# Performance work log

Hardware: AMD Instinct MI355X
Metric: run time of the kernel (lower is better)

Reference implementation:

```python
import jax, jax.numpy as jnp
import numpy as np

N = 30000      # nodes
E = 480000     # edges (before self-loops)
IN = 128       # in_dim
HID = 256      # hidden_dim
HEADS = 4
C = HID // HEADS  # per-head channels = 64
NEG_SLOPE = 0.2


def setup_inputs() -> dict:
    key = jax.random.key(0)
    ks = jax.random.split(key, 12)
    s_in = 1.0 / np.sqrt(IN)
    s_h = 1.0 / np.sqrt(HID)
    return {
        "x": jax.random.normal(ks[0], (N, IN), dtype=jnp.float32),
        "edge_index": jax.random.randint(ks[1], (2, E), 0, N, dtype=jnp.int32),
        # GAT layer 1 (in: IN -> HEADS*C)
        "W1": jax.random.normal(ks[2], (IN, HID), dtype=jnp.float32) * s_in,
        "att_src1": jax.random.normal(ks[3], (HEADS, C), dtype=jnp.float32) * s_h,
        "att_dst1": jax.random.normal(ks[4], (HEADS, C), dtype=jnp.float32) * s_h,
        "b1": jnp.zeros((HID,), dtype=jnp.float32),
        # GAT layer 2 (in: HID -> HEADS*C)
        "W2": jax.random.normal(ks[5], (HID, HID), dtype=jnp.float32) * s_h,
        "att_src2": jax.random.normal(ks[6], (HEADS, C), dtype=jnp.float32) * s_h,
        "att_dst2": jax.random.normal(ks[7], (HEADS, C), dtype=jnp.float32) * s_h,
        "b2": jnp.zeros((HID,), dtype=jnp.float32),
        # LayerNorms
        "g1": jnp.ones((HID,), dtype=jnp.float32),
        "be1": jnp.zeros((HID,), dtype=jnp.float32),
        "g2": jnp.ones((HID,), dtype=jnp.float32),
        "be2": jnp.zeros((HID,), dtype=jnp.float32),
        # residual projection (in_dim != hidden_dim)
        "Wp": jax.random.normal(ks[8], (IN, HID), dtype=jnp.float32) * s_in,
        "bp": jnp.zeros((HID,), dtype=jnp.float32),
    }


def layer_norm(x, g, b, eps=1e-5):
    mu = jnp.mean(x, axis=-1, keepdims=True)
    var = jnp.var(x, axis=-1, keepdims=True)
    return (x - mu) * jax.lax.rsqrt(var + eps) * g + b


def gat_conv(x, src, dst, W, a_src, a_dst, bias):
    """PyG-style GATConv (concat heads). src/dst already include self-loops."""
    n = x.shape[0]
    h = (x @ W).reshape(n, HEADS, C)                     # (N, H, C)
    e_src = jnp.sum(h * a_src, axis=-1)                  # (N, H)
    e_dst = jnp.sum(h * a_dst, axis=-1)                  # (N, H)
    e = jax.nn.leaky_relu(e_src[src] + e_dst[dst], NEG_SLOPE)  # (Etot, H)
    # per-destination segment softmax (numerically stable)
    e_max = jax.lax.stop_gradient(jax.ops.segment_max(e, dst, num_segments=n))
    p = jnp.exp(e - e_max[dst])
    denom = jax.ops.segment_sum(p, dst, num_segments=n)[dst]
    alpha = p / denom                                    # (Etot, H)
    out = jax.ops.segment_sum(h[src] * alpha[..., None], dst, num_segments=n)
    return out.reshape(n, HID) + bias


def reference(x, edge_index, W1, att_src1, att_dst1, b1, W2, att_src2, att_dst2, b2,
              g1, be1, g2, be2, Wp, bp):
    n = x.shape[0]
    loop = jnp.arange(n, dtype=edge_index.dtype)
    src = jnp.concatenate([edge_index[0], loop])
    dst = jnp.concatenate([edge_index[1], loop])

    residual = x @ Wp + bp                               # proj residual
    h = gat_conv(x, src, dst, W1, att_src1, att_dst1, b1)
    h = jax.nn.elu(layer_norm(h + residual, g1, be1))
    # dropout is identity at inference
    residual = h
    h2 = gat_conv(h, src, dst, W2, att_src2, att_dst2, b2)
    out = jax.nn.elu(layer_norm(h2 + residual, g2, be2))
    return out
```

## Files before the change

kernel.cpp:

```cpp
#include <hip/hip_runtime.h>
#include <cstdint>
#include <cstddef>

#define N_NODES 30000
#define E_EDGES 480000
#define ETOT    510000
#define IN_DIM  128
#define HID     256
#define HEADS   4
#define NEG_SLOPE 0.2f
#define DEG_BLOCKS 1993
#define GEMM1_BX 235

static inline int cdiv(int a, int b){ return (a + b - 1) / b; }

typedef short bf16x8 __attribute__((ext_vector_type(8)));
typedef float f32x4  __attribute__((ext_vector_type(4)));
typedef float f32x2  __attribute__((ext_vector_type(2)));

__device__ __forceinline__ unsigned short f2bf(float f) {
  unsigned u = __float_as_uint(f);
  unsigned r = (u + 0x7FFFu + ((u >> 16) & 1u)) >> 16;
  return (unsigned short)r;
}
__device__ __forceinline__ float bf2f(unsigned short s) {
  return __uint_as_float((unsigned)s << 16);
}
__device__ __forceinline__ unsigned char f2fp8(float v) {
  return (unsigned char)(__builtin_amdgcn_cvt_pk_fp8_f32(v, v, 0, false) & 0xFF);
}

__global__ __launch_bounds__(256) void zero_deg(int4* __restrict__ deg4)
{
  deg4[blockIdx.x * 256 + threadIdx.x] = int4{0, 0, 0, 0};
}

__global__ __launch_bounds__(256) void setup(
    const int* __restrict__ ei, int* __restrict__ deg,
    const float* __restrict__ x, const float* __restrict__ W1,
    const float* __restrict__ Wp, const float* __restrict__ W2,
    ushort* __restrict__ xbf, ushort* __restrict__ w1t,
    ushort* __restrict__ wpt, ushort* __restrict__ w2t)
{
  int b = blockIdx.x;
  int t = threadIdx.x;
  if (b < DEG_BLOCKS) {
    int e = b * 256 + t;
    if (e < ETOT) {
      int d = (e < E_EDGES) ? ei[E_EDGES + e] : (e - E_EDGES);
      atomicAdd(&deg[d], 1);
    }
    return;
  }
  b -= DEG_BLOCKS;
  if (b < 3750) {
    int i = b * 256 + t;
    float4 v = ((const float4*)x)[i];
    ushort4 o;
    o.x = f2bf(v.x); o.y = f2bf(v.y); o.z = f2bf(v.z); o.w = f2bf(v.w);
    ((ushort4*)xbf)[i] = o;
  } else if (b < 3750 + 128) {
    int k = b - 3750;
    w1t[(size_t)t * IN_DIM + k] = f2bf(W1[(size_t)k * HID + t]);
  } else if (b < 3750 + 256) {
    int k = b - 3878;
    wpt[(size_t)t * IN_DIM + k] = f2bf(Wp[(size_t)k * HID + t]);
  } else {
    int k = b - 4006;
    w2t[(size_t)t * HID + k] = f2bf(W2[(size_t)k * HID + t]);
  }
}

template<int K, bool L1>
__device__ __forceinline__ void gemm_body(
    int bx, int by,
    const ushort* __restrict__ A,
    const ushort* __restrict__ WT,
    const float* __restrict__ att_src, const float* __restrict__ att_dst,
    unsigned char* __restrict__ hout, float* __restrict__ esrc, float* __restrict__ edst,
    ushort* __restrict__ rout, const float* __restrict__ pbias, int n)
{
  const int wave = threadIdx.x >> 6;
  const int lane = threadIdx.x & 63;
  const int wr = wave >> 1, wc = wave & 1;
  const int brow = bx * 128 + wr * 64;
  const int bcol = by * 128 + wc * 64;
  const int lrow = lane & 15;
  const int kgrp = lane >> 4;

  f32x4 acc[4][4] = {};
  for (int k0 = 0; k0 < K; k0 += 32) {
    const int kb = k0 + kgrp * 8;
    bf16x8 a[4], b[4];
    #pragma unroll
    for (int mi = 0; mi < 4; ++mi) {
      int r = brow + mi * 16 + lrow;
      r = min(r, n - 1);
      a[mi] = *(const bf16x8*)&A[(size_t)r * K + kb];
    }
    #pragma unroll
    for (int ni = 0; ni < 4; ++ni) {
      int c = bcol + ni * 16 + lrow;
      b[ni] = *(const bf16x8*)&WT[(size_t)c * K + kb];
    }
    #pragma unroll
    for (int mi = 0; mi < 4; ++mi)
      #pragma unroll
      for (int ni = 0; ni < 4; ++ni)
        acc[mi][ni] = __builtin_amdgcn_mfma_f32_16x16x32_bf16(a[mi], b[ni], acc[mi][ni], 0, 0, 0);
  }
  const bool proj = L1 && (bcol >= 256);
  #pragma unroll
  for (int mi = 0; mi < 4; ++mi) {
    #pragma unroll
    for (int r = 0; r < 4; ++r) {
      int row = brow + mi * 16 + kgrp * 4 + r;
      if (row < n) {
        #pragma unroll
        for (int ni = 0; ni < 4; ++ni) {
          int colg = bcol + ni * 16 + lrow;
          float v = acc[mi][ni][r];
          if (proj) {
            int c = colg - 256;
            rout[(size_t)row * HID + c] = f2bf(v + pbias[c]);
          } else {
            hout[(size_t)row * HID + colg] = f2fp8(v);
          }
        }
      }
    }
  }
  if (!proj) {
    const int hh = bcol >> 6;
    float as[4], ad[4];
    #pragma unroll
    for (int ni = 0; ni < 4; ++ni) {
      as[ni] = att_src[hh * 64 + ni * 16 + lrow];
      ad[ni] = att_dst[hh * 64 + ni * 16 + lrow];
    }
    #pragma unroll
    for (int mi = 0; mi < 4; ++mi) {
      #pragma unroll
      for (int r = 0; r < 4; ++r) {
        float vs = 0.f, vd = 0.f;
        #pragma unroll
        for (int ni = 0; ni < 4; ++ni) {
          float c = acc[mi][ni][r];
          vs += c * as[ni];
          vd += c * ad[ni];
        }
        #pragma unroll
        for (int m = 1; m <= 8; m <<= 1) {
          vs += __shfl_xor(vs, m);
          vd += __shfl_xor(vd, m);
        }
        int row = brow + mi * 16 + kgrp * 4 + r;
        if (lrow == 0 && row < n) {
          esrc[row * HEADS + hh] = vs;
          edst[row * HEADS + hh] = vd;
        }
      }
    }
  }
}

__global__ __launch_bounds__(256) void gemm1_scatter(
    const int* __restrict__ ei, int* __restrict__ cursor, int* __restrict__ col,
    const ushort* __restrict__ A, const ushort* __restrict__ WT,
    const float* __restrict__ att_src, const float* __restrict__ att_dst,
    unsigned char* __restrict__ hout, float* __restrict__ esrc,
    float* __restrict__ edst, ushort* __restrict__ rout,
    const float* __restrict__ pbias, int n)
{
  int b = blockIdx.x;
  if (b < DEG_BLOCKS) {
    int e = b * 256 + threadIdx.x;
    if (e < ETOT) {
      int s, d;
      if (e < E_EDGES) { s = ei[e]; d = ei[E_EDGES + e]; }
      else             { s = d = e - E_EDGES; }
      int pos = atomicAdd(&cursor[d], 1);
      col[pos] = s;
    }
    return;
  }
  b -= DEG_BLOCKS;
  gemm_body<IN_DIM, true>(b % GEMM1_BX, b / GEMM1_BX,
                          A, WT, att_src, att_dst, hout, esrc, edst, rout, pbias, n);
}

__global__ __launch_bounds__(256) void gemm2(
    const ushort* __restrict__ A, const ushort* __restrict__ WT,
    const float* __restrict__ att_src, const float* __restrict__ att_dst,
    unsigned char* __restrict__ hout, float* __restrict__ esrc,
    float* __restrict__ edst, int n)
{
  gemm_body<HID, false>(blockIdx.x, blockIdx.y,
                        A, WT, att_src, att_dst, hout, esrc, edst, nullptr, nullptr, n);
}

__global__ __launch_bounds__(1024) void scan_rowptr(const int* __restrict__ deg,
                                                    int* __restrict__ rowptr,
                                                    int* __restrict__ cursor)
{
  const int CE = 30;
  __shared__ int wtot[16];
  __shared__ int wexc[16];
  int t = threadIdx.x;
  int wv = t >> 6, lane = t & 63;
  int base = t * CE;
  int local[CE];
  int s = 0;
  #pragma unroll
  for (int i = 0; i < CE; ++i) {
    int idx = base + i;
    int v = (idx < N_NODES) ? deg[idx] : 0;
    local[i] = s;
    s += v;
  }
  int incl = s;
  #pragma unroll
  for (int off = 1; off < 64; off <<= 1) {
    int v = __shfl_up(incl, off);
    if (lane >= off) incl += v;
  }
  if (lane == 63) wtot[wv] = incl;
  __syncthreads();
  if (t < 16) {
    int v = wtot[t];
    int inc2 = v;
    #pragma unroll
    for (int off = 1; off < 16; off <<= 1) {
      int u = __shfl_up(inc2, off);
      if (t >= off) inc2 += u;
    }
    wexc[t] = inc2 - v;
  }
  __syncthreads();
  int off0 = wexc[wv] + (incl - s);
  #pragma unroll
  for (int i = 0; i < CE; ++i) {
    int idx = base + i;
    if (idx < N_NODES) {
      rowptr[idx] = off0 + local[i];
      cursor[idx] = off0 + local[i];
    }
  }
  if (t == 1023) rowptr[N_NODES] = off0 + s;
}

template<bool WRITE_BF16>
__global__ __launch_bounds__(256) void gat_agg(
    const int* __restrict__ rowptr, const int* __restrict__ col,
    const float* __restrict__ esrc, const float* __restrict__ edst,
    const unsigned char* __restrict__ h8, const float* __restrict__ bias,
    const ushort* __restrict__ resid, const float* __restrict__ gamma,
    const float* __restrict__ beta, float* __restrict__ out_f32,
    ushort* __restrict__ out_bf16)
{
  const int t = threadIdx.x;
  const int lane16 = t & 15;
  const int d = blockIdx.x * 16 + (t >> 4);
  const int cblk = lane16 * 16;
  const int headc = lane16 >> 2;
  const int r0 = rowptr[d], r1 = rowptr[d + 1];

  const uint4* rp = (const uint4*)&resid[(size_t)d * HID + cblk];
  uint4 r0v = rp[0], r1v = rp[1];
  const float edh = edst[d * HEADS + headc];

  f32x2 acc2[8] = {};
  float dp = 0.f;

  for (int j = r0; j < r1; j += 8) {
    int s[8];
    #pragma unroll
    for (int i = 0; i < 8; ++i) s[i] = col[min(j + i, r1 - 1)];
    float es[8];
    #pragma unroll
    for (int i = 0; i < 8; ++i) es[i] = esrc[s[i] * HEADS + headc];
    uint4 w[8];
    #pragma unroll
    for (int i = 0; i < 8; ++i)
      w[i] = *(const uint4*)&h8[(size_t)s[i] * HID + cblk];
    #pragma unroll
    for (int i = 0; i < 8; ++i) {
      float v = es[i] + edh;
      v = (v >= 0.f) ? v : NEG_SLOPE * v;
      float p = (j + i < r1) ? __expf(v) : 0.f;
      dp += p;
      f32x2 p2 = { p, p };
      unsigned wd0 = w[i].x, wd1 = w[i].y, wd2 = w[i].z, wd3 = w[i].w;
      acc2[0] += __builtin_amdgcn_cvt_pk_f32_fp8(wd0, false) * p2;
      acc2[1] += __builtin_amdgcn_cvt_pk_f32_fp8(wd0, true)  * p2;
      acc2[2] += __builtin_amdgcn_cvt_pk_f32_fp8(wd1, false) * p2;
      acc2[3] += __builtin_amdgcn_cvt_pk_f32_fp8(wd1, true)  * p2;
      acc2[4] += __builtin_amdgcn_cvt_pk_f32_fp8(wd2, false) * p2;
      acc2[5] += __builtin_amdgcn_cvt_pk_f32_fp8(wd2, true)  * p2;
      acc2[6] += __builtin_amdgcn_cvt_pk_f32_fp8(wd3, false) * p2;
      acc2[7] += __builtin_amdgcn_cvt_pk_f32_fp8(wd3, true)  * p2;
    }
  }

  float rden = 1.f / dp;

  f32x2 v2[8];
  {
    unsigned rd[8] = { r0v.x, r0v.y, r0v.z, r0v.w, r1v.x, r1v.y, r1v.z, r1v.w };
    const f32x2* b2 = (const f32x2*)&bias[cblk];
    f32x2 rden2 = { rden, rden };
    #pragma unroll
    for (int q = 0; q < 8; ++q) {
      f32x2 rw;
      rw.x = __uint_as_float(rd[q] << 16);
      rw.y = __uint_as_float(rd[q] & 0xffff0000u);
      v2[q] = acc2[q] * rden2 + b2[q] + rw;
    }
  }

  float s1 = 0.f, s2 = 0.f;
  #pragma unroll
  for (int q = 0; q < 8; ++q) {
    s1 += v2[q].x + v2[q].y;
    s2 += v2[q].x * v2[q].x + v2[q].y * v2[q].y;
  }
  #pragma unroll
  for (int m = 1; m <= 8; m <<= 1) {
    s1 += __shfl_xor(s1, m);
    s2 += __shfl_xor(s2, m);
  }
  float mu = s1 * (1.f / HID);
  float var = s2 * (1.f / HID) - mu * mu;
  float rr = rsqrtf(var + 1e-5f);

  const f32x2* g2 = (const f32x2*)&gamma[cblk];
  const f32x2* e2 = (const f32x2*)&beta[cblk];
  float y[16];
  #pragma unroll
  for (int q = 0; q < 8; ++q) {
    f32x2 g = g2[q], e = e2[q];
    float t0 = (v2[q].x - mu) * rr * g.x + e.x;
    float t1 = (v2[q].y - mu) * rr * g.y + e.y;
    y[2 * q]     = (t0 > 0.f) ? t0 : expm1f(t0);
    y[2 * q + 1] = (t1 > 0.f) ? t1 : expm1f(t1);
  }
  if (WRITE_BF16) {
    uint4 o[2];
    #pragma unroll
    for (int q = 0; q < 8; ++q) {
      unsigned wv = (unsigned)f2bf(y[2 * q]) | ((unsigned)f2bf(y[2 * q + 1]) << 16);
      ((unsigned*)o)[q] = wv;
    }
    uint4* op = (uint4*)&out_bf16[(size_t)d * HID + cblk];
    op[0] = o[0]; op[1] = o[1];
  } else {
    float4* op = (float4*)&out_f32[(size_t)d * HID + cblk];
    #pragma unroll
    for (int q = 0; q < 4; ++q) {
      float4 ov = { y[4 * q], y[4 * q + 1], y[4 * q + 2], y[4 * q + 3] };
      op[q] = ov;
    }
  }
}

extern "C" void kernel_launch(void* const* d_in, const int* in_sizes, int n_in,
                              void* d_out, int out_size, void* d_ws, size_t ws_size,
                              hipStream_t stream) {
  const float* x   = (const float*)d_in[0];
  const int*   ei  = (const int*)d_in[1];
  const float* W1  = (const float*)d_in[2];
  const float* as1 = (const float*)d_in[3];
  const float* ad1 = (const float*)d_in[4];
  const float* b1  = (const float*)d_in[5];
  const float* W2  = (const float*)d_in[6];
  const float* as2 = (const float*)d_in[7];
  const float* ad2 = (const float*)d_in[8];
  const float* b2  = (const float*)d_in[9];
  const float* g1  = (const float*)d_in[10];
  const float* be1 = (const float*)d_in[11];
  const float* g2  = (const float*)d_in[12];
  const float* be2 = (const float*)d_in[13];
  const float* Wp  = (const float*)d_in[14];
  const float* bp  = (const float*)d_in[15];
  float* out = (float*)d_out;

  const size_t NB16 = (size_t)N_NODES * HID * sizeof(ushort);
  const size_t NB8  = (size_t)N_NODES * HID;
  const size_t XB16 = (size_t)N_NODES * IN_DIM * sizeof(ushort);
  const size_t NH_BUF = (size_t)N_NODES * HEADS * sizeof(float);
  char* ws = (char*)d_ws;
  size_t off = 0;
  unsigned char* h8 = (unsigned char*)(ws + off); off += NB8;
  ushort* hAbf  = (ushort*)(ws + off); off += NB16;
  ushort* rbf   = (ushort*)(ws + off); off += NB16;
  ushort* xbf   = (ushort*)(ws + off); off += XB16;
  ushort* w1t   = (ushort*)(ws + off); off += (size_t)HID * IN_DIM * 2;
  ushort* wpt   = (ushort*)(ws + off); off += (size_t)HID * IN_DIM * 2;
  ushort* w2t   = (ushort*)(ws + off); off += (size_t)HID * HID * 2;
  float*  esrc  = (float*) (ws + off); off += NH_BUF;
  float*  edstb = (float*) (ws + off); off += NH_BUF;
  int*    deg    = (int*)(ws + off); off += (size_t)30720 * 4;
  int*    rowptr = (int*)(ws + off); off += (size_t)(N_NODES + 1) * 4;
  int*    cursor = (int*)(ws + off); off += (size_t)N_NODES * 4;
  int*    col    = (int*)(ws + off); off += (size_t)ETOT * 4;

  zero_deg<<<30, 256, 0, stream>>>((int4*)deg);
  setup<<<DEG_BLOCKS + 3750 + 128 + 128 + 256, 256, 0, stream>>>(
      ei, deg, x, W1, Wp, W2, xbf, w1t, wpt, w2t);
  scan_rowptr<<<1, 1024, 0, stream>>>(deg, rowptr, cursor);

  gemm1_scatter<<<DEG_BLOCKS + GEMM1_BX * 4, 256, 0, stream>>>(
      ei, cursor, col, xbf, w1t, as1, ad1, h8, esrc, edstb, rbf, bp, N_NODES);
  gat_agg<true><<<N_NODES / 16, 256, 0, stream>>>(
      rowptr, col, esrc, edstb, h8, b1, rbf, g1, be1, nullptr, hAbf);

  gemm2<<<dim3(GEMM1_BX, 2), 256, 0, stream>>>(
      hAbf, w2t, as2, ad2, h8, esrc, edstb, N_NODES);
  gat_agg<false><<<N_NODES / 16, 256, 0, stream>>>(
      rowptr, col, esrc, edstb, h8, b2, hAbf, g2, be2, out, nullptr);
}
```

Before: 217.8 us.

## Stage GEMM tiles in LDS via direct global-to-LDS loads and split scatter kernel

Measured after the change: 207.1 us. 4.9% less time.

```diff
diff --git a/kernel.cpp b/kernel.cpp
--- a/kernel.cpp
+++ b/kernel.cpp
@@ -10,7 +10,6 @@
 #define HEADS   4
 #define NEG_SLOPE 0.2f
 #define DEG_BLOCKS 1993
-#define GEMM1_BX 235
 
 static inline int cdiv(int a, int b){ return (a + b - 1) / b; }
 
@@ -28,6 +27,11 @@
 }
 __device__ __forceinline__ unsigned char f2fp8(float v) {
   return (unsigned char)(__builtin_amdgcn_cvt_pk_fp8_f32(v, v, 0, false) & 0xFF);
+}
+__device__ __forceinline__ void gload_lds16(const void* g, void* l) {
+  __builtin_amdgcn_global_load_lds(
+      (const __attribute__((address_space(1))) void*)g,
+      (__attribute__((address_space(3))) void*)l, 16, 0, 0);
 }
 
 __global__ __launch_bounds__(256) void zero_deg(int4* __restrict__ deg4)
@@ -71,50 +75,138 @@
   }
 }
 
+__global__ __launch_bounds__(1024) void scan_rowptr(const int* __restrict__ deg,
+                                                    int* __restrict__ rowptr,
+                                                    int* __restrict__ cursor)
+{
+  const int CE = 30;
+  __shared__ int wtot[16];
+  __shared__ int wexc[16];
+  int t = threadIdx.x;
+  int wv = t >> 6, lane = t & 63;
+  int base = t * CE;
+  int local[CE];
+  int s = 0;
+  #pragma unroll
+  for (int i = 0; i < CE; ++i) {
+    int idx = base + i;
+    int v = (idx < N_NODES) ? deg[idx] : 0;
+    local[i] = s;
+    s += v;
+  }
+  int incl = s;
+  #pragma unroll
+  for (int off = 1; off < 64; off <<= 1) {
+    int v = __shfl_up(incl, off);
+    if (lane >= off) incl += v;
+  }
+  if (lane == 63) wtot[wv] = incl;
+  __syncthreads();
+  if (t < 16) {
+    int v = wtot[t];
+    int inc2 = v;
+    #pragma unroll
+    for (int off = 1; off < 16; off <<= 1) {
+      int u = __shfl_up(inc2, off);
+      if (t >= off) inc2 += u;
+    }
+    wexc[t] = inc2 - v;
+  }
+  __syncthreads();
+  int off0 = wexc[wv] + (incl - s);
+  #pragma unroll
+  for (int i = 0; i < CE; ++i) {
+    int idx = base + i;
+    if (idx < N_NODES) {
+      rowptr[idx] = off0 + local[i];
+      cursor[idx] = off0 + local[i];
+    }
+  }
+  if (t == 1023) rowptr[N_NODES] = off0 + s;
+}
+
+__global__ __launch_bounds__(256) void scatter_edges(const int* __restrict__ ei,
+                                                     int* __restrict__ cursor,
+                                                     int* __restrict__ col)
+{
+  int e = blockIdx.x * blockDim.x + threadIdx.x;
+  if (e >= ETOT) return;
+  int s, d;
+  if (e < E_EDGES) { s = ei[e]; d = ei[E_EDGES + e]; }
+  else             { s = d = e - E_EDGES; }
+  int pos = atomicAdd(&cursor[d], 1);
+  col[pos] = s;
+}
+
 template<int K, bool L1>
-__device__ __forceinline__ void gemm_body(
-    int bx, int by,
+__global__ __launch_bounds__(256) void gemm_lds(
     const ushort* __restrict__ A,
     const ushort* __restrict__ WT,
     const float* __restrict__ att_src, const float* __restrict__ att_dst,
-    unsigned char* __restrict__ hout, float* __restrict__ esrc, float* __restrict__ edst,
-    ushort* __restrict__ rout, const float* __restrict__ pbias, int n)
-{
-  const int wave = threadIdx.x >> 6;
-  const int lane = threadIdx.x & 63;
-  const int wr = wave >> 1, wc = wave & 1;
-  const int brow = bx * 128 + wr * 64;
-  const int bcol = by * 128 + wc * 64;
+    unsigned char* __restrict__ hout, float* __restrict__ esrc,
+    float* __restrict__ edst, ushort* __restrict__ rout,
+    const float* __restrict__ pbias, int n)
+{
+  __shared__ ushort As[128 * 32];
+  __shared__ ushort Bs[128 * 32];
+  const int t = threadIdx.x;
+  const int wv = t >> 6;
+  const int lane = t & 63;
+  const int wr = wv >> 1, wc = wv & 1;
+  const int brow = blockIdx.x * 128;
+  const int bcol0 = blockIdx.y * 128;
   const int lrow = lane & 15;
   const int kgrp = lane >> 4;
 
+  int sc_row[2], sc_kc[2];
+  #pragma unroll
+  for (int i = 0; i < 2; ++i) {
+    int chunk = wv * 128 + i * 64 + lane;
+    sc_row[i] = chunk >> 2;
+    sc_kc[i] = (chunk & 3) ^ (sc_row[i] & 3);
+  }
+
   f32x4 acc[4][4] = {};
   for (int k0 = 0; k0 < K; k0 += 32) {
-    const int kb = k0 + kgrp * 8;
+    #pragma unroll
+    for (int i = 0; i < 2; ++i) {
+      int ar = min(brow + sc_row[i], n - 1);
+      gload_lds16(&A[(size_t)ar * K + k0 + sc_kc[i] * 8],
+                  &As[(size_t)(wv * 2 + i) * 512]);
+      int bc = bcol0 + sc_row[i];
+      gload_lds16(&WT[(size_t)bc * K + k0 + sc_kc[i] * 8],
+                  &Bs[(size_t)(wv * 2 + i) * 512]);
+    }
+    __syncthreads();
     bf16x8 a[4], b[4];
     #pragma unroll
     for (int mi = 0; mi < 4; ++mi) {
-      int r = brow + mi * 16 + lrow;
-      r = min(r, n - 1);
-      a[mi] = *(const bf16x8*)&A[(size_t)r * K + kb];
+      int tr = wr * 64 + mi * 16 + lrow;
+      int pos = kgrp ^ (tr & 3);
+      a[mi] = *(const bf16x8*)&As[tr * 32 + pos * 8];
     }
     #pragma unroll
     for (int ni = 0; ni < 4; ++ni) {
-      int c = bcol + ni * 16 + lrow;
-      b[ni] = *(const bf16x8*)&WT[(size_t)c * K + kb];
+      int tc = wc * 64 + ni * 16 + lrow;
+      int pos = kgrp ^ (tc & 3);
+      b[ni] = *(const bf16x8*)&Bs[tc * 32 + pos * 8];
     }
     #pragma unroll
     for (int mi = 0; mi < 4; ++mi)
       #pragma unroll
       for (int ni = 0; ni < 4; ++ni)
         acc[mi][ni] = __builtin_amdgcn_mfma_f32_16x16x32_bf16(a[mi], b[ni], acc[mi][ni], 0, 0, 0);
-  }
+    __syncthreads();
+  }
+
+  const int bcol = bcol0 + wc * 64;
   const bool proj = L1 && (bcol >= 256);
+  const int browt = brow + wr * 64;
   #pragma unroll
   for (int mi = 0; mi < 4; ++mi) {
     #pragma unroll
     for (int r = 0; r < 4; ++r) {
-      int row = brow + mi * 16 + kgrp * 4 + r;
+      int row = browt + mi * 16 + kgrp * 4 + r;
       if (row < n) {
         #pragma unroll
         for (int ni = 0; ni < 4; ++ni) {
@@ -154,7 +246,7 @@
           vs += __shfl_xor(vs, m);
           vd += __shfl_xor(vd, m);
         }
-        int row = brow + mi * 16 + kgrp * 4 + r;
+        int row = browt + mi * 16 + kgrp * 4 + r;
         if (lrow == 0 && row < n) {
           esrc[row * HEADS + hh] = vs;
           edst[row * HEADS + hh] = vd;
@@ -162,91 +254,6 @@
       }
     }
   }
-}
-
-__global__ __launch_bounds__(256) void gemm1_scatter(
-    const int* __restrict__ ei, int* __restrict__ cursor, int* __restrict__ col,
-    const ushort* __restrict__ A, const ushort* __restrict__ WT,
-    const float* __restrict__ att_src, const float* __restrict__ att_dst,
-    unsigned char* __restrict__ hout, float* __restrict__ esrc,
-    float* __restrict__ edst, ushort* __restrict__ rout,
-    const float* __restrict__ pbias, int n)
-{
-  int b = blockIdx.x;
-  if (b < DEG_BLOCKS) {
-    int e = b * 256 + threadIdx.x;
-    if (e < ETOT) {
-      int s, d;
-      if (e < E_EDGES) { s = ei[e]; d = ei[E_EDGES + e]; }
-      else             { s = d = e - E_EDGES; }
-      int pos = atomicAdd(&cursor[d], 1);
-      col[pos] = s;
-    }
-    return;
-  }
-  b -= DEG_BLOCKS;
-  gemm_body<IN_DIM, true>(b % GEMM1_BX, b / GEMM1_BX,
-                          A, WT, att_src, att_dst, hout, esrc, edst, rout, pbias, n);
-}
-
-__global__ __launch_bounds__(256) void gemm2(
-    const ushort* __restrict__ A, const ushort* __restrict__ WT,
-    const float* __restrict__ att_src, const float* __restrict__ att_dst,
-    unsigned char* __restrict__ hout, float* __restrict__ esrc,
-    float* __restrict__ edst, int n)
-{
-  gemm_body<HID, false>(blockIdx.x, blockIdx.y,
-                        A, WT, att_src, att_dst, hout, esrc, edst, nullptr, nullptr, n);
-}
-
-__global__ __launch_bounds__(1024) void scan_rowptr(const int* __restrict__ deg,
-                                                    int* __restrict__ rowptr,
-                                                    int* __restrict__ cursor)
-{
-  const int CE = 30;
-  __shared__ int wtot[16];
-  __shared__ int wexc[16];
-  int t = threadIdx.x;
-  int wv = t >> 6, lane = t & 63;
-  int base = t * CE;
-  int local[CE];
-  int s = 0;
-  #pragma unroll
-  for (int i = 0; i < CE; ++i) {
-    int idx = base + i;
-    int v = (idx < N_NODES) ? deg[idx] : 0;
-    local[i] = s;
-    s += v;
-  }
-  int incl = s;
-  #pragma unroll
-  for (int off = 1; off < 64; off <<= 1) {
-    int v = __shfl_up(incl, off);
-    if (lane >= off) incl += v;
-  }
-  if (lane == 63) wtot[wv] = incl;
-  __syncthreads();
-  if (t < 16) {
-    int v = wtot[t];
-    int inc2 = v;
-    #pragma unroll
-    for (int off = 1; off < 16; off <<= 1) {
-      int u = __shfl_up(inc2, off);
-      if (t >= off) inc2 += u;
-    }
-    wexc[t] = inc2 - v;
-  }
-  __syncthreads();
-  int off0 = wexc[wv] + (incl - s);
-  #pragma unroll
-  for (int i = 0; i < CE; ++i) {
-    int idx = base + i;
-    if (idx < N_NODES) {
-      rowptr[idx] = off0 + local[i];
-      cursor[idx] = off0 + local[i];
-    }
-  }
-  if (t == 1023) rowptr[N_NODES] = off0 + s;
 }
 
 template<bool WRITE_BF16>
@@ -408,14 +415,15 @@
   setup<<<DEG_BLOCKS + 3750 + 128 + 128 + 256, 256, 0, stream>>>(
       ei, deg, x, W1, Wp, W2, xbf, w1t, wpt, w2t);
   scan_rowptr<<<1, 1024, 0, stream>>>(deg, rowptr, cursor);
-
-  gemm1_scatter<<<DEG_BLOCKS + GEMM1_BX * 4, 256, 0, stream>>>(
-      ei, cursor, col, xbf, w1t, as1, ad1, h8, esrc, edstb, rbf, bp, N_NODES);
+  scatter_edges<<<cdiv(ETOT, 256), 256, 0, stream>>>(ei, cursor, col);
+
+  gemm_lds<IN_DIM, true><<<dim3(cdiv(N_NODES, 128), 4), 256, 0, stream>>>(
+      xbf, w1t, as1, ad1, h8, esrc, edstb, rbf, bp, N_NODES);
   gat_agg<true><<<N_NODES / 16, 256, 0, stream>>>(
       rowptr, col, esrc, edstb, h8, b1, rbf, g1, be1, nullptr, hAbf);
 
-  gemm2<<<dim3(GEMM1_BX, 2), 256, 0, stream>>>(
-      hAbf, w2t, as2, ad2, h8, esrc, edstb, N_NODES);
+  gemm_lds<HID, false><<<dim3(cdiv(N_NODES, 128), 2), 256, 0, stream>>>(
+      hAbf, w2t, as2, ad2, h8, esrc, edstb, nullptr, nullptr, N_NODES);
   gat_agg<false><<<N_NODES / 16, 256, 0, stream>>>(
       rowptr, col, esrc, edstb, h8, b2, hAbf, g2, be2, out, nullptr);
 }
```
